# Optimization experiments

Measured on AMD Instinct MI355X. Metric: run time of the kernel, lower is better.

## Reference

```python
import jax, jax.numpy as jnp
import numpy as np

B, N, D, N_HOPS = 32, 1024, 128, 3
EPS = 1e-6


def setup_inputs() -> dict:
    key = jax.random.key(0)
    k1, k2, k3, k4 = jax.random.split(key, 4)
    # binary base adjacency (non-trainable buffer in the torch module)
    adj = (jax.random.uniform(k1, (N, N)) < 0.05).astype(jnp.float32)
    adj_weight = jax.random.uniform(k2, (B, N, N), dtype=jnp.float32)
    x = jax.random.normal(k3, (B, N, D), dtype=jnp.float32)
    W = jax.random.normal(k4, (D, D), dtype=jnp.float32) * 0.05
    b = jnp.zeros((D,), jnp.float32)
    a2 = jnp.ones((D,), jnp.float32)   # LayerNorm scale
    b2 = jnp.zeros((D,), jnp.float32)  # LayerNorm shift
    return {"x": x, "adj_weight": adj_weight, "adj": adj, "W": W, "b": b, "a2": a2, "b2": b2}


def _conv(x, adj_weight, adj):
    # adj_power squares the matrix each hop: hop h uses A^(2^h).
    # mask_h = (A^(2^h) == 1.0); weighted hop = (W^(2^h)) * mask_h.
    # propagate(edge_index from dense_to_sparse) == sum_j Wmask[b,j,i] * x[b,j]  (A^T x)
    A = adj            # [N, N]
    Wp = adj_weight    # [B, N, N]
    agg = jnp.zeros_like(x)
    for h in range(N_HOPS):
        mask = (A == 1.0).astype(x.dtype)          # [N, N]
        Wh = Wp * mask                              # [B, N, N]
        agg = agg + jnp.einsum('bji,bjd->bid', Wh, x)
        if h < N_HOPS - 1:
            A = A @ A
            Wp = jnp.matmul(Wp, Wp)
    return agg


def reference(x, adj_weight, adj, W, b, a2, b2):
    agg = _conv(x, adj_weight, adj)
    h = jnp.einsum('bnd,od->bno', agg, W) + b + x   # Linear + residual
    mean = jnp.mean(h, axis=-1, keepdims=True)
    std = jnp.std(h, axis=-1, keepdims=True, ddof=1)  # torch.std is unbiased
    y = a2 * (h - mean) / (std + EPS) + b2
    return y  # dropout p=0 (eval) -> identity
```

## Files before the change

### kernel.cpp

```cpp
#include <hip/hip_runtime.h>

#define NN 1024
#define BB 32
#define DD 128
#define EPSF 1e-6f
#define CAP 16384
#define NNNN ((size_t)NN * NN)

typedef __bf16 bf16x8 __attribute__((ext_vector_type(8)));
typedef float  f32x4  __attribute__((ext_vector_type(4)));
typedef unsigned short u16x8 __attribute__((ext_vector_type(8)));

__device__ __forceinline__ float bf2f(unsigned short u) {
  union { unsigned int i; float f; } v; v.i = ((unsigned int)u) << 16; return v.f;
}
__device__ __forceinline__ unsigned short f2bf(float f) {
  union { float f; unsigned int i; } v; v.f = f;
  unsigned int r = v.i + 0x7fffu + ((v.i >> 16) & 1u);
  return (unsigned short)(r >> 16);
}


__global__ __launch_bounds__(256) void convert_wp(const float* __restrict__ src,
    unsigned short* __restrict__ Wp, unsigned short* __restrict__ WpT) {
  __shared__ float tile[64][65];
  const int b = blockIdx.z;
  const int c0 = blockIdx.x * 64, r0 = blockIdx.y * 64;
  const int t = threadIdx.x;
  const int rr = t >> 3, cb = (t & 7) * 8;
  const size_t base = (size_t)b * NNNN;
#pragma unroll
  for (int p = 0; p < 2; ++p) {
    const int r = rr + p * 32;
    const float* srow = src + base + (size_t)(r0 + r) * NN + c0 + cb;
    f32x4 v0 = *(const f32x4*)srow;
    f32x4 v1 = *(const f32x4*)(srow + 4);
    u16x8 w;
#pragma unroll
    for (int j = 0; j < 4; ++j) { w[j] = f2bf(v0[j]); w[4 + j] = f2bf(v1[j]); }
    *(u16x8*)(Wp + base + (size_t)(r0 + r) * NN + c0 + cb) = w;
#pragma unroll
    for (int j = 0; j < 4; ++j) { tile[r][cb + j] = v0[j]; tile[r][cb + 4 + j] = v1[j]; }
  }
  __syncthreads();
#pragma unroll
  for (int p = 0; p < 2; ++p) {
    const int r = rr + p * 32;
    u16x8 w;
#pragma unroll
    for (int j = 0; j < 8; ++j) w[j] = f2bf(tile[cb + j][r]);
    *(u16x8*)(WpT + base + (size_t)(c0 + r) * NN + r0 + cb) = w;
  }
}

__global__ __launch_bounds__(256) void convert_x(const float* __restrict__ x,
    unsigned short* __restrict__ xT) {
  __shared__ float tile[32][33];
  const int b = blockIdx.z;
  const int d0 = blockIdx.x * 32, n0 = blockIdx.y * 32;
  const int tx = threadIdx.x, ty = threadIdx.y;
#pragma unroll
  for (int s = 0; s < 4; ++s) {
    int rr = ty + s * 8;
    tile[rr][tx] = x[(size_t)b * NN * DD + (size_t)(n0 + rr) * DD + d0 + tx];
  }
  __syncthreads();
#pragma unroll
  for (int s = 0; s < 4; ++s) {
    int rr = ty + s * 8;
    xT[(size_t)b * DD * NN + (size_t)(d0 + rr) * NN + n0 + tx] = f2bf(tile[tx][rr]);
  }
}

__global__ __launch_bounds__(256) void mask0cvt(const float* __restrict__ adj,
    unsigned char* __restrict__ mcode, unsigned short* __restrict__ adjbf,
    unsigned short* __restrict__ adjTbf) {
  __shared__ float tile[32][33];
  const int i0 = blockIdx.x * 32, j0 = blockIdx.y * 32;
  const int tx = threadIdx.x, ty = threadIdx.y;
#pragma unroll
  for (int s = 0; s < 4; ++s) {
    int rr = ty + s * 8;
    float v = adj[(size_t)(j0 + rr) * NN + i0 + tx];
    adjbf[(size_t)(j0 + rr) * NN + i0 + tx] = f2bf(v);
    tile[rr][tx] = v;
  }
  __syncthreads();
#pragma unroll
  for (int s = 0; s < 4; ++s) {
    int rr = ty + s * 8;
    float v = tile[tx][rr];
    adjTbf[(size_t)(i0 + rr) * NN + j0 + tx] = f2bf(v);
    mcode[(size_t)(i0 + rr) * NN + j0 + tx] = (v == 1.0f) ? 1 : 0;
  }
}

__global__ __launch_bounds__(256) void scan_a2(const float* __restrict__ P,
    unsigned short* __restrict__ A2, unsigned short* __restrict__ A2T,
    unsigned char* __restrict__ mcode) {
  __shared__ float tile[32][33];
  const int m0 = blockIdx.x * 32, n0 = blockIdx.y * 32;
  const int tx = threadIdx.x, ty = threadIdx.y;
#pragma unroll
  for (int s = 0; s < 4; ++s) {
    int rr = ty + s * 8;
    size_t idx = (size_t)(m0 + rr) * NN + n0 + tx;
    float v = P[idx] + P[NNNN + idx] + P[2 * NNNN + idx] + P[3 * NNNN + idx];
    A2[idx] = f2bf(v);
    tile[rr][tx] = v;
  }
  __syncthreads();
#pragma unroll
  for (int s = 0; s < 4; ++s) {
    int rr = ty + s * 8;
    float v = tile[tx][rr];
    A2T[(size_t)(n0 + rr) * NN + m0 + tx] = f2bf(v);
    if (v == 1.0f) mcode[(size_t)(n0 + rr) * NN + m0 + tx] |= 2;
  }
}

__global__ __launch_bounds__(256) void scan_a4(const float* __restrict__ P,
    unsigned int* __restrict__ entries, int* __restrict__ nnz) {
  size_t e = (size_t)blockIdx.x * 256 + threadIdx.x;
  float v = P[e] + P[NNNN + e] + P[2 * NNNN + e] + P[3 * NNNN + e];
  if (v == 1.0f) {
    int idx = atomicAdd(nnz, 1);
    if (idx < CAP) entries[idx] = ((unsigned)(e >> 10) << 16) | (unsigned)(e & 1023);
  }
}

#define BM 128
#define BN 128
#define BK 32

struct EpiWcomb {
  const unsigned char* mc;
  unsigned short* out;
  __device__ __forceinline__ void operator()(int b, int ks, int i, int j, float v) const {
    size_t idx = (size_t)i * NN + j;
    out[(size_t)b * NNNN + idx] = (mc[idx] & 2) ? f2bf(v) : (unsigned short)0;
  }
};

struct EpiSqPart {
  float* buf;
  __device__ __forceinline__ void operator()(int b, int ks, int i, int j, float v) const {
    buf[(size_t)ks * NNNN + (size_t)i * NN + j] = v;
  }
};

struct EpiAggPart {
  float* p0;
  float* p1;
  __device__ __forceinline__ void operator()(int b, int ks, int i, int d, float v) const {
    (ks ? p1 : p0)[(size_t)b * NN * DD + (size_t)i * DD + d] = v;
  }
};

#define LGKM_BARRIER() do { \
  asm volatile("s_waitcnt lgkmcnt(0)" ::: "memory"); \
  __builtin_amdgcn_s_barrier(); \
  asm volatile("" ::: "memory"); } while (0)

template <int MW, bool COMB, typename Epi>
__global__ __launch_bounds__(256, MW) void gemm_pipe(
    const unsigned short* __restrict__ Ap, size_t sA,
    const unsigned short* __restrict__ WtP, const unsigned char* __restrict__ McP,
    const unsigned short* __restrict__ Bp, size_t sB,
    int swz, int ksN, int nit, Epi epi) {
  __shared__ __align__(16) unsigned short As[2 * BM * BK];
  __shared__ __align__(16) unsigned short Bs[2 * BN * BK];
  const int z = blockIdx.z;
  const int b = z / ksN, ks = z - b * ksN;
  const int kbase = ks * nit * BK;
  int bx = blockIdx.x, by = blockIdx.y;
  if (swz) {
    int lin = bx + (by << 3);
    int r = lin & 7, s = lin >> 3;
    bx = ((r & 3) << 1) | (s & 1);
    by = ((r >> 2) << 2) | (s >> 1);
  }
  const int tm = bx * BM, tn = by * BN;
  const unsigned short* Ab = Ap + (size_t)b * sA;
  const unsigned short* Bb = Bp + (size_t)b * sB;
  const unsigned short* Wb = COMB ? (WtP + (size_t)b * sA) : nullptr;
  const int tid = threadIdx.x;
  const int w = tid >> 6, l = tid & 63;
  const int lr = l >> 2, lc = l & 3;
  const int fr = l & 15, quad = l >> 4;
  const int moff = (w & 1) * 64, noff = (w >> 1) * 64;
  const int r0 = w * 16 + lr, r1 = (w + 4) * 16 + lr;
  const int kc0 = lc ^ ((r0 >> 1) & 3), kc1 = lc ^ ((r1 >> 1) & 3);
  const size_t ao0 = (size_t)(tm + r0) * NN + kbase + kc0 * 8;
  const size_t ao1 = (size_t)(tm + r1) * NN + kbase + kc1 * 8;
  const size_t bo0 = (size_t)(tn + r0) * NN + kbase + kc0 * 8;
  const size_t bo1 = (size_t)(tn + r1) * NN + kbase + kc1 * 8;
  const int ls0 = r0 * BK + lc * 8, ls1 = r1 * BK + lc * 8;

  unsigned short* const As0 = As;           unsigned short* const As1 = As + BM * BK;
  unsigned short* const Bs0 = Bs;           unsigned short* const Bs1 = Bs + BN * BK;

  f32x4 acc[4][4];
#pragma unroll
  for (int mi = 0; mi < 4; ++mi)
#pragma unroll
    for (int ni = 0; ni < 4; ++ni) acc[mi][ni] = (f32x4){0.f, 0.f, 0.f, 0.f};

  struct RegSet {
    u16x8 a0, a1, b0, b1;
    u16x8 w0, w1;
    unsigned long long m0, m1;
  };
  RegSet R0, R1;

  auto load = [&](RegSet& R, int kt) {
    size_t kk = (size_t)kt * BK;
    R.a0 = *(const u16x8*)(Ab + ao0 + kk);
    R.a1 = *(const u16x8*)(Ab + ao1 + kk);
    R.b0 = *(const u16x8*)(Bb + bo0 + kk);
    R.b1 = *(const u16x8*)(Bb + bo1 + kk);
    if constexpr (COMB) {
      R.w0 = *(const u16x8*)(Wb + ao0 + kk);
      R.w1 = *(const u16x8*)(Wb + ao1 + kk);
      R.m0 = *(const unsigned long long*)(McP + ao0 + kk);
      R.m1 = *(const unsigned long long*)(McP + ao1 + kk);
    }
  };
  auto wr = [&](const RegSet& R, unsigned short* Ad, unsigned short* Bd) {
    if constexpr (COMB) {
      u16x8 f0, f1;
#pragma unroll
      for (int j = 0; j < 8; ++j) {
        float s0 = bf2f(R.a0[j]);
        if ((R.m0 >> (8 * j)) & 1ull) s0 += bf2f(R.w0[j]);
        f0[j] = f2bf(s0);
        float s1 = bf2f(R.a1[j]);
        if ((R.m1 >> (8 * j)) & 1ull) s1 += bf2f(R.w1[j]);
        f1[j] = f2bf(s1);
      }
      *(u16x8*)(Ad + ls0) = f0;
      *(u16x8*)(Ad + ls1) = f1;
    } else {
      *(u16x8*)(Ad + ls0) = R.a0;
      *(u16x8*)(Ad + ls1) = R.a1;
    }
    *(u16x8*)(Bd + ls0) = R.b0;
    *(u16x8*)(Bd + ls1) = R.b1;
  };
  auto compute = [&](const unsigned short* Ad, const unsigned short* Bd) {
    bf16x8 af[4], bfr[4];
#pragma unroll
    for (int mi = 0; mi < 4; ++mi) {
      int r = moff + mi * 16 + fr;
      int kc = quad ^ ((r >> 1) & 3);
      af[mi] = *(const bf16x8*)(Ad + r * BK + kc * 8);
    }
#pragma unroll
    for (int ni = 0; ni < 4; ++ni) {
      int r = noff + ni * 16 + fr;
      int kc = quad ^ ((r >> 1) & 3);
      bfr[ni] = *(const bf16x8*)(Bd + r * BK + kc * 8);
    }
#pragma unroll
    for (int mi = 0; mi < 4; ++mi)
#pragma unroll
      for (int ni = 0; ni < 4; ++ni)
        acc[mi][ni] = __builtin_amdgcn_mfma_f32_16x16x32_bf16(af[mi], bfr[ni], acc[mi][ni], 0, 0, 0);
  };

  load(R0, 0);
  load(R1, 1);
  wr(R0, As0, Bs0);
  load(R0, 2);
  LGKM_BARRIER();
#pragma unroll 1
  for (int kt = 0; kt < nit - 2; kt += 2) {
    compute(As0, Bs0);
    wr(R1, As1, Bs1);
    if (kt + 3 < nit) load(R1, kt + 3);
    LGKM_BARRIER();
    compute(As1, Bs1);
    wr(R0, As0, Bs0);
    if (kt + 4 < nit) load(R0, kt + 4);
    LGKM_BARRIER();
  }
  compute(As0, Bs0);
  wr(R1, As1, Bs1);
  LGKM_BARRIER();
  compute(As1, Bs1);

#pragma unroll
  for (int mi = 0; mi < 4; ++mi)
#pragma unroll
    for (int ni = 0; ni < 4; ++ni)
#pragma unroll
      for (int t = 0; t < 4; ++t)
        epi(b, ks, tm + moff + mi * 16 + quad * 4 + t, tn + noff + ni * 16 + fr, acc[mi][ni][t]);
}

__global__ __launch_bounds__(256) void hop2_fix(const unsigned short* __restrict__ Wp,
    const unsigned short* __restrict__ WpT, const int* __restrict__ nnz,
    const unsigned int* __restrict__ entries, unsigned short* __restrict__ WcombT) {
  int n = *nnz;
  if (n > CAP) n = CAP;
  if (n == 0) return;
  __shared__ float rbuf[256];
  const int b = blockIdx.x;
  const size_t bnn = (size_t)b * NNNN;
  for (int e = blockIdx.y; e < n; e += gridDim.y) {
    unsigned int ent = entries[e];
    int j = ent >> 16, i = ent & 0xFFFF;
    float s = 0.f;
    for (int k = threadIdx.x; k < NN; k += 256) {
      float u = 0.f, v = 0.f;
      const unsigned short* wj  = Wp  + bnn + (size_t)j * NN;
      const unsigned short* wtk = WpT + bnn + (size_t)k * NN;
      const unsigned short* wk  = Wp  + bnn + (size_t)k * NN;
      const unsigned short* wti = WpT + bnn + (size_t)i * NN;
      for (int t = 0; t < NN; ++t) {
        u += bf2f(wj[t]) * bf2f(wtk[t]);
        v += bf2f(wk[t]) * bf2f(wti[t]);
      }
      s += u * v;
    }
    rbuf[threadIdx.x] = s;
    __syncthreads();
    for (int off = 128; off > 0; off >>= 1) {
      if (threadIdx.x < off) rbuf[threadIdx.x] += rbuf[threadIdx.x + off];
      __syncthreads();
    }
    if (threadIdx.x == 0) {
      size_t idx = bnn + (size_t)i * NN + j;
      WcombT[idx] = f2bf(bf2f(WcombT[idx]) + rbuf[0]);
    }
    __syncthreads();
  }
}

#define FROWS 16
__global__ __launch_bounds__(256) void fused_out(const float* __restrict__ a0p,
    const float* __restrict__ a1p, const float* __restrict__ x,
    const float* __restrict__ W, const float* __restrict__ bias,
    const float* __restrict__ g2, const float* __restrict__ bsh,
    float* __restrict__ out) {
  __shared__ unsigned short Wl[128 * 136];
  __shared__ float ar[256];
  __shared__ float wred[8];
  const int tid = threadIdx.x;
  for (int e = tid; e < 16384; e += 256) Wl[(e >> 7) * 136 + (e & 127)] = f2bf(W[e]);
  const int half = tid >> 7, o = tid & 127;
  const int w = tid >> 6, lane = tid & 63;
  const float bo = bias[o], go = g2[o], b2o = bsh[o];
  const size_t row0 = (size_t)blockIdx.x * FROWS;
  size_t rb = row0 * DD;
  float av = a0p[rb + tid] + a1p[rb + tid];
  float xv = x[rb + tid];
  __syncthreads();
  for (int rr = 0; rr < FROWS; rr += 2) {
    ar[tid] = av;
    const float xcur = xv;
    const size_t rbc = (row0 + rr) * DD;
    __syncthreads();
    if (rr + 2 < FROWS) {
      size_t rb2 = (row0 + rr + 2) * DD;
      av = a0p[rb2 + tid] + a1p[rb2 + tid];
      xv = x[rb2 + tid];
    }
    float hv = bo + xcur;
    const unsigned short* wrow = &Wl[o * 136];
    const float* arow = &ar[half * 128];
#pragma unroll
    for (int d8 = 0; d8 < 16; ++d8) {
      bf16x8 wv = *(const bf16x8*)(wrow + d8 * 8);
#pragma unroll
      for (int t = 0; t < 8; ++t) hv += (float)wv[t] * arow[d8 * 8 + t];
    }
    float s = hv, q = hv * hv;
#pragma unroll
    for (int off = 32; off > 0; off >>= 1) {
      s += __shfl_xor(s, off);
      q += __shfl_xor(q, off);
    }
    if (lane == 0) { wred[w] = s; wred[4 + w] = q; }
    __syncthreads();
    float st = wred[half * 2] + wred[half * 2 + 1];
    float qt = wred[4 + half * 2] + wred[4 + half * 2 + 1];
    float mean = st * (1.0f / 128.0f);
    float var = (qt - 128.0f * mean * mean) * (1.0f / 127.0f);
    var = fmaxf(var, 0.0f);
    float stdv = sqrtf(var);
    out[rbc + tid] = go * (hv - mean) / (stdv + EPSF) + b2o;
  }
}

extern "C" void kernel_launch(void* const* d_in, const int* in_sizes, int n_in,
                              void* d_out, int out_size, void* d_ws, size_t ws_size,
                              hipStream_t stream) {
  (void)in_sizes; (void)n_in; (void)out_size; (void)ws_size;
  const float* x    = (const float*)d_in[0];
  const float* adjw = (const float*)d_in[1];
  const float* adj  = (const float*)d_in[2];
  const float* W    = (const float*)d_in[3];
  const float* bias = (const float*)d_in[4];
  const float* a2   = (const float*)d_in[5];
  const float* b2   = (const float*)d_in[6];
  float* out = (float*)d_out;

  char* ws = (char*)d_ws;
  const size_t MB = 1048576;
  unsigned short* Wp_bf   = (unsigned short*)(ws);
  unsigned short* WpT_bf  = (unsigned short*)(ws + 64 * MB);
  unsigned short* WcombT  = (unsigned short*)(ws + 128 * MB);
  unsigned short* xT_bf   = (unsigned short*)(ws + 192 * MB);
  unsigned short* adj_bf  = (unsigned short*)(ws + 200 * MB);
  unsigned short* adjT_bf = (unsigned short*)(ws + 202 * MB);
  unsigned short* A2_bf   = (unsigned short*)(ws + 204 * MB);
  unsigned short* A2T_bf  = (unsigned short*)(ws + 206 * MB);
  float* sqpart           = (float*)(ws + 208 * MB);
  float* agg1             = (float*)(ws + 200 * MB);
  unsigned char* mcode    = (unsigned char*)(ws + 224 * MB);
  unsigned int* entries   = (unsigned int*)(ws + 225 * MB);
  int* nnz2               = (int*)(ws + 226 * MB);
  float* agg0 = out;

  hipMemsetAsync(nnz2, 0, 4, stream);

  dim3 blk32(32, 8, 1);
  convert_wp<<<dim3(16, 16, 32), 256, 0, stream>>>(adjw, Wp_bf, WpT_bf);
  convert_x<<<dim3(4, 32, 32), blk32, 0, stream>>>(x, xT_bf);
  mask0cvt<<<dim3(32, 32, 1), blk32, 0, stream>>>(adj, mcode, adj_bf, adjT_bf);

  gemm_pipe<3, false><<<dim3(8, 8, 4), 256, 0, stream>>>(
      adj_bf, (size_t)0, nullptr, nullptr, adjT_bf, (size_t)0, 0, 4, 8,
      EpiSqPart{sqpart});
  scan_a2<<<dim3(32, 32, 1), blk32, 0, stream>>>(sqpart, A2_bf, A2T_bf, mcode);
  gemm_pipe<3, false><<<dim3(8, 8, 4), 256, 0, stream>>>(
      A2_bf, (size_t)0, nullptr, nullptr, A2T_bf, (size_t)0, 0, 4, 8,
      EpiSqPart{sqpart});
  scan_a4<<<dim3(4096, 1, 1), 256, 0, stream>>>(sqpart, entries, nnz2);

  gemm_pipe<3, false><<<dim3(8, 8, 32), 256, 0, stream>>>(
      WpT_bf, NNNN, nullptr, nullptr, Wp_bf, NNNN, 1, 1, NN / BK,
      EpiWcomb{mcode, WcombT});

  hop2_fix<<<dim3(32, 8, 1), 256, 0, stream>>>(Wp_bf, WpT_bf, nnz2, entries, WcombT);

  gemm_pipe<2, true><<<dim3(8, 1, 64), 256, 0, stream>>>(
      WcombT, NNNN, WpT_bf, mcode, xT_bf, (size_t)DD * NN, 0, 2, 16,
      EpiAggPart{agg0, agg1});

  fused_out<<<dim3(2048, 1, 1), 256, 0, stream>>>(agg0, agg1, x, W, bias, a2, b2, out);
}
```

Baseline: 473.0 us.

## Add direct global-to-LDS GEMM kernel for adjacency and weight squaring

Adds a new GEMM kernel that loads A and B tiles straight into LDS with global_load_lds, using an XOR-swizzled layout and a single LDS buffer. It replaces the register-staged double-buffered gemm_pipe for the two adjacency-squaring GEMMs and the batched Wp·Wp GEMM. The aim is to cut VGPR pressure and LDS write instructions so occupancy can rise (launch bound 4). The trade-off is that load and compute no longer overlap, since each iteration has to wait on a barrier before any MFMA work starts.

```diff
diff --git a/kernel.cpp b/kernel.cpp
--- a/kernel.cpp
+++ b/kernel.cpp
@@ -10,6 +10,16 @@
 typedef __bf16 bf16x8 __attribute__((ext_vector_type(8)));
 typedef float  f32x4  __attribute__((ext_vector_type(4)));
 typedef unsigned short u16x8 __attribute__((ext_vector_type(8)));
+
+typedef __attribute__((address_space(3))) unsigned int lds_u32;
+typedef __attribute__((address_space(1))) const unsigned int glb_u32;
+
+__device__ __forceinline__ lds_u32* lds_cast(const void* p) {
+  return (lds_u32*)(unsigned int)(unsigned long long)p;
+}
+__device__ __forceinline__ glb_u32* glb_cast(const void* p) {
+  return (glb_u32*)(unsigned long long)p;
+}
 
 __device__ __forceinline__ float bf2f(unsigned short u) {
   union { unsigned int i; float f; } v; v.i = ((unsigned int)u) << 16; return v.f;
@@ -161,6 +171,89 @@
   asm volatile("s_waitcnt lgkmcnt(0)" ::: "memory"); \
   __builtin_amdgcn_s_barrier(); \
   asm volatile("" ::: "memory"); } while (0)
+
+template <int MW, typename Epi>
+__global__ __launch_bounds__(256, MW) void gemm_lds(
+    const unsigned short* __restrict__ Ap, size_t sA,
+    const unsigned short* __restrict__ Bp, size_t sB,
+    int swz, int ksN, int nit, Epi epi) {
+  __shared__ __align__(16) unsigned short As[BM * BK];
+  __shared__ __align__(16) unsigned short Bs[BN * BK];
+  const int z = blockIdx.z;
+  const int b = z / ksN, ks = z - b * ksN;
+  const int kbase = ks * nit * BK;
+  int bx = blockIdx.x, by = blockIdx.y;
+  if (swz) {
+    int lin = bx + (by << 3);
+    int r = lin & 7, s = lin >> 3;
+    bx = ((r & 3) << 1) | (s & 1);
+    by = ((r >> 2) << 2) | (s >> 1);
+  }
+  const int tm = bx * BM, tn = by * BN;
+  const unsigned short* Ab = Ap + (size_t)b * sA;
+  const unsigned short* Bb = Bp + (size_t)b * sB;
+  const int tid = threadIdx.x;
+  const int w = tid >> 6, l = tid & 63;
+  const int fr = l & 15, quad = l >> 4;
+  const int moff = (w & 1) * 64, noff = (w >> 1) * 64;
+
+  const int sr = l >> 2, ss = l & 3;
+  const int r0 = w * 16 + sr;
+  const int r1 = 64 + w * 16 + sr;
+  const int kc0 = ss ^ ((r0 >> 1) & 3);
+  const int kc1 = ss ^ ((r1 >> 1) & 3);
+  const unsigned short* gA0 = Ab + (size_t)(tm + r0) * NN + kbase + kc0 * 8;
+  const unsigned short* gA1 = Ab + (size_t)(tm + r1) * NN + kbase + kc1 * 8;
+  const unsigned short* gB0 = Bb + (size_t)(tn + r0) * NN + kbase + kc0 * 8;
+  const unsigned short* gB1 = Bb + (size_t)(tn + r1) * NN + kbase + kc1 * 8;
+  lds_u32* const lA0 = lds_cast(As + (w * 16) * BK);
+  lds_u32* const lA1 = lds_cast(As + (64 + w * 16) * BK);
+  lds_u32* const lB0 = lds_cast(Bs + (w * 16) * BK);
+  lds_u32* const lB1 = lds_cast(Bs + (64 + w * 16) * BK);
+
+  f32x4 acc[4][4];
+#pragma unroll
+  for (int mi = 0; mi < 4; ++mi)
+#pragma unroll
+    for (int ni = 0; ni < 4; ++ni) acc[mi][ni] = (f32x4){0.f, 0.f, 0.f, 0.f};
+
+#pragma unroll 1
+  for (int kt = 0; kt < nit; ++kt) {
+    const size_t kk = (size_t)kt * BK;
+    __builtin_amdgcn_global_load_lds(glb_cast(gA0 + kk), lA0, 16, 0, 0);
+    __builtin_amdgcn_global_load_lds(glb_cast(gA1 + kk), lA1, 16, 0, 0);
+    __builtin_amdgcn_global_load_lds(glb_cast(gB0 + kk), lB0, 16, 0, 0);
+    __builtin_amdgcn_global_load_lds(glb_cast(gB1 + kk), lB1, 16, 0, 0);
+    __syncthreads();
+    bf16x8 af[4], bfr[4];
+#pragma unroll
+    for (int mi = 0; mi < 4; ++mi) {
+      int r = moff + mi * 16 + fr;
+      int kc = quad ^ ((r >> 1) & 3);
+      af[mi] = *(const bf16x8*)(As + r * BK + kc * 8);
+    }
+#pragma unroll
+    for (int ni = 0; ni < 4; ++ni) {
+      int r = noff + ni * 16 + fr;
+      int kc = quad ^ ((r >> 1) & 3);
+      bfr[ni] = *(const bf16x8*)(Bs + r * BK + kc * 8);
+    }
+#pragma unroll
+    for (int mi = 0; mi < 4; ++mi)
+#pragma unroll
+      for (int ni = 0; ni < 4; ++ni)
+        acc[mi][ni] = __builtin_amdgcn_mfma_f32_16x16x32_bf16(af[mi], bfr[ni], acc[mi][ni], 0, 0, 0);
+    __syncthreads();
+  }
+
+#pragma unroll
+  for (int mi = 0; mi < 4; ++mi)
+#pragma unroll
+    for (int ni = 0; ni < 4; ++ni)
+#pragma unroll
+      for (int t = 0; t < 4; ++t)
+        epi(b, ks, tm + moff + mi * 16 + quad * 4 + t, tn + noff + ni * 16 + fr, acc[mi][ni][t]);
+}
 
 template <int MW, bool COMB, typename Epi>
 __global__ __launch_bounds__(256, MW) void gemm_pipe(
@@ -430,18 +523,15 @@
   convert_x<<<dim3(4, 32, 32), blk32, 0, stream>>>(x, xT_bf);
   mask0cvt<<<dim3(32, 32, 1), blk32, 0, stream>>>(adj, mcode, adj_bf, adjT_bf);
 
-  gemm_pipe<3, false><<<dim3(8, 8, 4), 256, 0, stream>>>(
-      adj_bf, (size_t)0, nullptr, nullptr, adjT_bf, (size_t)0, 0, 4, 8,
-      EpiSqPart{sqpart});
+  gemm_lds<4><<<dim3(8, 8, 4), 256, 0, stream>>>(
+      adj_bf, (size_t)0, adjT_bf, (size_t)0, 0, 4, 8, EpiSqPart{sqpart});
   scan_a2<<<dim3(32, 32, 1), blk32, 0, stream>>>(sqpart, A2_bf, A2T_bf, mcode);
-  gemm_pipe<3, false><<<dim3(8, 8, 4), 256, 0, stream>>>(
-      A2_bf, (size_t)0, nullptr, nullptr, A2T_bf, (size_t)0, 0, 4, 8,
-      EpiSqPart{sqpart});
+  gemm_lds<4><<<dim3(8, 8, 4), 256, 0, stream>>>(
+      A2_bf, (size_t)0, A2T_bf, (size_t)0, 0, 4, 8, EpiSqPart{sqpart});
   scan_a4<<<dim3(4096, 1, 1), 256, 0, stream>>>(sqpart, entries, nnz2);
 
-  gemm_pipe<3, false><<<dim3(8, 8, 32), 256, 0, stream>>>(
-      WpT_bf, NNNN, nullptr, nullptr, Wp_bf, NNNN, 1, 1, NN / BK,
-      EpiWcomb{mcode, WcombT});
+  gemm_lds<4><<<dim3(8, 8, 32), 256, 0, stream>>>(
+      WpT_bf, NNNN, Wp_bf, NNNN, 1, 1, NN / BK, EpiWcomb{mcode, WcombT});
 
   hop2_fix<<<dim3(32, 8, 1), 256, 0, stream>>>(Wp_bf, WpT_bf, nnz2, entries, WcombT);
 
```

Result: no change. 478.7 us (+1.2%).
